# Kernel optimization log

Hardware: AMD Instinct MI355X
Metric: run time of the kernel (lower is better)

Reference implementation:

```python
import jax, jax.numpy as jnp
import numpy as np

B, NX, W, DX, DY, D, H, P = 8, 512, 16, 1536, 1024, 768, 12, 8


def setup_inputs() -> dict:
    key = jax.random.key(0)
    ks = jax.random.split(key, 12)
    r = lambda k, s: jax.random.normal(k, s, dtype=jnp.float32) * 0.02
    return {
        "x": jax.random.normal(ks[0], (B, NX, DX), jnp.float32),
        "y": jax.random.normal(ks[1], (B, NX * W, DY), jnp.float32),
        "Wx": r(ks[2], (DX, D)), "bx": jnp.zeros((D,), jnp.float32),
        "Wy": r(ks[3], (DY, D)), "by": jnp.zeros((D,), jnp.float32),
        "prompt": r(ks[4], (1, P, D)),
        "Wq": r(ks[5], (D, D)), "bq": jnp.zeros((D,), jnp.float32),
        "Wk": r(ks[6], (D, D)), "bk": jnp.zeros((D,), jnp.float32),
        "Wv": r(ks[7], (D, D)), "bv": jnp.zeros((D,), jnp.float32),
        "Wo": r(ks[8], (D, D)), "bo": jnp.zeros((D,), jnp.float32),
        "ln_g": jnp.ones((D,), jnp.float32), "ln_b": jnp.zeros((D,), jnp.float32),
    }


def _l2n(f, eps=1e-6):
    return f / (jnp.linalg.norm(f, axis=-1, keepdims=True) + eps)


def reference(x, y, Wx, bx, Wy, by, prompt, Wq, bq, Wk, bk, Wv, bv, Wo, bo, ln_g, ln_b):
    dh = D // H
    scale = 1.0 / jnp.sqrt(jnp.float32(dh))
    xp = _l2n(x @ Wx + bx)            # [B,NX,D]
    yp = _l2n(y @ Wy + by)            # [B,NX*W,D]
    # In the original, only normalized_output[:,0:1] is kept per window, and
    # per-query attention is independent, so only query index 0 contributes.
    q = ((xp[:, 0] @ Wq) + bq).reshape(B, H, dh) * scale   # [B,H,dh]
    yw = yp.reshape(B, NX, W, D)                            # 16-token windows
    k = ((yw @ Wk) + bk).reshape(B, NX, W, H, dh)
    v = ((yw @ Wv) + bv).reshape(B, NX, W, H, dh)
    s = jnp.einsum('bhd,bnwhd->bhnw', q, k)                # [B,H,NX,W]
    a = jax.nn.softmax(s, axis=-1)
    ctx = jnp.einsum('bhnw,bnwhd->bnhd', a, v).reshape(B, NX, D)
    o = ctx @ Wo + bo                                      # attn out_proj
    mu = jnp.mean(o, axis=-1, keepdims=True)
    var = jnp.var(o, axis=-1, keepdims=True)
    normed = (o - mu) / jnp.sqrt(var + 1e-6) * ln_g + ln_b  # [B,NX,D]
    blocks = jnp.concatenate(
        [normed[:, :, None, :],
         jnp.broadcast_to(prompt[:, None], (B, NX, P, D))], axis=2)  # [B,NX,1+P,D]
    return blocks.reshape(B, NX * (1 + P), D)
```

## Files before the change

### kernel.cpp

```cpp
#include <hip/hip_runtime.h>
#include <stdint.h>

#define BQ 8
#define NXQ 512
#define WQ 16
#define DXQ 1536
#define DYQ 1024
#define DQ 768
#define HQ 12
#define PQ 8
#define MY 65536
#define BN_ROWS 4096

typedef __attribute__((ext_vector_type(8))) short short8;
typedef __attribute__((ext_vector_type(4))) float f32x4;
typedef unsigned short ushort_t;
typedef unsigned int uint_t;

__device__ __forceinline__ ushort_t f2bf(float f) {
  uint_t u = __float_as_uint(f);
  u += 0x7FFFu + ((u >> 16) & 1u);
  return (ushort_t)(u >> 16);
}
__device__ __forceinline__ float bf2f(ushort_t h) {
  return __uint_as_float(((uint_t)h) << 16);
}
__device__ __forceinline__ void gload_lds16(const void* g, void* l) {
  __builtin_amdgcn_global_load_lds(
      (__attribute__((address_space(1))) unsigned int*)(g),
      (__attribute__((address_space(3))) unsigned int*)(l), 16, 0, 0);
}

__global__ void k_conv(const float* __restrict__ y, const float* __restrict__ Wy,
                       const float* __restrict__ Wv, const float* __restrict__ Wo,
                       ushort_t* __restrict__ ybf, ushort_t* __restrict__ WyT,
                       ushort_t* __restrict__ WvT, ushort_t* __restrict__ WoT,
                       float* __restrict__ rowsq, float* __restrict__ oS12,
                       float* __restrict__ xw) {
  const int gstride = gridDim.x * blockDim.x;
  const int g0 = blockIdx.x * blockDim.x + threadIdx.x;
  const int NY8 = MY * DYQ / 8;
  for (int i = g0; i < NY8; i += gstride) {
    const float4* s = (const float4*)(y + (size_t)i * 8);
    float4 f0 = s[0], f1 = s[1];
    short8 hv;
    hv[0] = (short)f2bf(f0.x); hv[1] = (short)f2bf(f0.y);
    hv[2] = (short)f2bf(f0.z); hv[3] = (short)f2bf(f0.w);
    hv[4] = (short)f2bf(f1.x); hv[5] = (short)f2bf(f1.y);
    hv[6] = (short)f2bf(f1.z); hv[7] = (short)f2bf(f1.w);
    *(short8*)(ybf + (size_t)i * 8) = hv;
  }
  for (int i = g0; i < MY; i += gstride) rowsq[i] = 0.f;
  for (int i = g0; i < 2 * BN_ROWS; i += gstride) oS12[i] = 0.f;
  for (int i = g0; i < BQ * DQ; i += gstride) xw[i] = 0.f;
  const int N1 = DQ * DYQ;
  const int N2 = DQ * DQ;
  const int total = N1 + 2 * N2;
  for (int i = g0; i < total; i += gstride) {
    if (i < N1) {
      int n = i / DYQ, k = i - n * DYQ;
      WyT[i] = f2bf(Wy[k * DQ + n]);
    } else if (i < N1 + N2) {
      int j = i - N1;
      int n = j / DQ, k = j - n * DQ;
      WvT[j] = f2bf(Wv[k * DQ + n]);
    } else {
      int j = i - N1 - N2;
      int n = j / DQ, k = j - n * DQ;
      WoT[j] = f2bf(Wo[k * DQ + n]);
    }
  }
}

__global__ __launch_bounds__(128) void k_q1(const float* __restrict__ x,
                                            const float* __restrict__ Wx,
                                            const float* __restrict__ bx,
                                            float* __restrict__ xw) {
  const int b = blockIdx.x, c = blockIdx.y * 128 + threadIdx.x;
  const int kc = blockIdx.z;
  const float* xr = x + (size_t)b * NXQ * DXQ + kc * 192;
  const float* wp = Wx + (size_t)kc * 192 * DQ + c;
  float acc = (kc == 0) ? bx[c] : 0.f;
  for (int k = 0; k < 192; ++k) acc += xr[k] * wp[(size_t)k * DQ];
  atomicAdd(&xw[b * DQ + c], acc);
}

__global__ __launch_bounds__(128) void k_q2(const float* __restrict__ xw,
                                            const float* __restrict__ Wq,
                                            const float* __restrict__ bq,
                                            float* __restrict__ qv) {
  const int b = blockIdx.x, c = blockIdx.y * 128 + threadIdx.x;
  const float* xr = xw + b * DQ;
  float acc = 0.f, ss = 0.f;
  for (int k = 0; k < DQ; ++k) {
    float v = xr[k];
    acc += v * Wq[(size_t)k * DQ + c];
    ss += v * v;
  }
  const float inv = 1.0f / (sqrtf(ss) + 1e-6f);
  qv[b * DQ + c] = (acc * inv + bq[c]) * 0.125f;
}

__global__ void k_q3(const float* __restrict__ Wk, const float* __restrict__ bk,
                     const float* __restrict__ qv, float* __restrict__ qk,
                     float* __restrict__ cQ) {
  const int bh = blockIdx.x;
  const int b = bh / HQ, h = bh - b * HQ;
  const int tid = threadIdx.x;
  const float* q = qv + b * DQ + h * 64;
#pragma unroll
  for (int j = 0; j < 3; ++j) {
    int dd = tid + j * 256;
    float acc = 0.f;
    for (int j2 = 0; j2 < 64; ++j2) acc += Wk[(size_t)dd * DQ + h * 64 + j2] * q[j2];
    qk[(size_t)bh * DQ + dd] = acc;
  }
  if (tid == 0) {
    float acc = 0.f;
    for (int j2 = 0; j2 < 64; ++j2) acc += q[j2] * bk[h * 64 + j2];
    cQ[bh] = acc;
  }
}

__global__ __launch_bounds__(512, 1) void k_gemm_yp(const ushort_t* __restrict__ ybf,
                                                    const ushort_t* __restrict__ WyT,
                                                    const float* __restrict__ by,
                                                    ushort_t* __restrict__ z,
                                                    float* __restrict__ rowsqg) {
  __shared__ __align__(16) char smem[131072 + 1024];
  float* rowsq_l = (float*)(smem + 131072);
  const int tid = threadIdx.x, lane = tid & 63, wv = tid >> 6;
  const int wvM = wv >> 2, wvN = wv & 3;
  const int g = blockIdx.x;
  const int m = (g / 24) * 8 + (g & 7);
  const int n = (g >> 3) % 3;
  const int mBase = m * 256, nBase = n * 256;
  if (tid < 256) rowsq_l[tid] = 0.f;

  const int sr = lane >> 2;
  const int sc = (lane & 3) ^ ((lane >> 3) & 3);
  const ushort_t* aQ[2]; const ushort_t* bQ[2];
  int qDst[2];
#pragma unroll
  for (int j = 0; j < 2; ++j) {
    int r = wv * 32 + j * 16 + sr;
    aQ[j] = ybf + (size_t)(mBase + r) * DYQ + sc * 8;
    bQ[j] = WyT + (size_t)(nBase + r) * DYQ + sc * 8;
    qDst[j] = (wv * 32 + j * 16) * 64;
  }
  const int q = lane >> 4;
  const int fsw = ((lane & 15) >> 1) & 3;
  int aFr[8], bFr[4];
#pragma unroll
  for (int mf = 0; mf < 8; ++mf) {
    int r = wvM * 128 + mf * 16 + (lane & 15);
    aFr[mf] = r * 64 + ((q ^ fsw) << 4);
  }
#pragma unroll
  for (int nf = 0; nf < 4; ++nf) {
    int r = wvN * 64 + nf * 16 + (lane & 15);
    bFr[nf] = 16384 + r * 64 + ((q ^ fsw) << 4);
  }

#define YP_STAGE(pp)                                                           \
  {                                                                            \
    char* db = smem + ((pp) & 3) * 32768;                                      \
    const int koff = ((pp) >> 1) * 64 + ((pp) & 1) * 32;                       \
    _Pragma("unroll") for (int j = 0; j < 2; ++j)                              \
        gload_lds16(aQ[j] + koff, db + qDst[j]);                               \
    _Pragma("unroll") for (int j = 0; j < 2; ++j)                              \
        gload_lds16(bQ[j] + koff, db + 16384 + qDst[j]);                       \
  }

  f32x4 acc[8][4] = {};
  YP_STAGE(0);
  YP_STAGE(1);
  YP_STAGE(2);
  asm volatile("s_waitcnt vmcnt(8)" ::: "memory");
  __builtin_amdgcn_s_barrier();
  __builtin_amdgcn_sched_barrier(0);

  for (int t = 0; t < 16; ++t) {
#pragma unroll
    for (int ks = 0; ks < 2; ++ks) {
      const int p = 2 * t + ks;
      const char* cb = smem + (p & 3) * 32768;
      short8 af[8], bf[4];
#pragma unroll
      for (int mf = 0; mf < 8; ++mf) af[mf] = *(const short8*)(cb + aFr[mf]);
#pragma unroll
      for (int nf = 0; nf < 4; ++nf) bf[nf] = *(const short8*)(cb + bFr[nf]);
      if (p <= 28) YP_STAGE(p + 3);
      asm volatile("s_waitcnt lgkmcnt(0)" ::: "memory");
      __builtin_amdgcn_sched_barrier(0);
      __builtin_amdgcn_s_setprio(1);
#pragma unroll
      for (int nf = 0; nf < 4; ++nf)
#pragma unroll
        for (int mf = 0; mf < 8; ++mf)
          acc[mf][nf] = __builtin_amdgcn_mfma_f32_16x16x32_bf16(af[mf], bf[nf],
                                                                acc[mf][nf], 0, 0, 0);
      __builtin_amdgcn_s_setprio(0);
      __builtin_amdgcn_sched_barrier(0);
      if (p <= 28) {
        asm volatile("s_waitcnt vmcnt(8)" ::: "memory");
      } else if (p == 29) {
        asm volatile("s_waitcnt vmcnt(4)" ::: "memory");
      } else {
        asm volatile("s_waitcnt vmcnt(0)" ::: "memory");
      }
      __builtin_amdgcn_s_barrier();
      __builtin_amdgcn_sched_barrier(0);
    }
  }
  __syncthreads();

  float byv[4];
#pragma unroll
  for (int nf = 0; nf < 4; ++nf) byv[nf] = by[nBase + wvN * 64 + nf * 16 + (lane & 15)];
#pragma unroll
  for (int mf = 0; mf < 8; ++mf) {
#pragma unroll
    for (int rr = 0; rr < 4; ++rr) {
      int row_l = wvM * 128 + mf * 16 + (lane >> 4) * 4 + rr;
      float ss = 0.f;
#pragma unroll
      for (int nf = 0; nf < 4; ++nf) {
        float zv = acc[mf][nf][rr] + byv[nf];
        ss += zv * zv;
        int col_l = wvN * 64 + nf * 16 + (lane & 15);
        *(ushort_t*)(smem + row_l * 512 + col_l * 2) = f2bf(zv);
      }
#pragma unroll
      for (int o = 1; o < 16; o <<= 1) ss += __shfl_xor(ss, o, 64);
      if ((lane & 15) == 0) atomicAdd(&rowsq_l[row_l], ss);
    }
  }
  __syncthreads();
  if (tid < 256) atomicAdd(&rowsqg[mBase + tid], rowsq_l[tid]);
#pragma unroll
  for (int it = 0; it < 16; ++it) {
    int row = it * 16 + (tid >> 5);
    int ch = tid & 31;
    uint4 v = *(const uint4*)(smem + row * 512 + ch * 16);
    *(uint4*)(z + (size_t)(mBase + row) * DQ + nBase + ch * 8) = v;
  }
}

__global__ __launch_bounds__(256) void k_attn(const ushort_t* __restrict__ z,
                                              const float* __restrict__ rowsqg,
                                              const float* __restrict__ qk,
                                              const float* __restrict__ cQ,
                                              ushort_t* __restrict__ p) {
  __shared__ __align__(16) char smem[16 * 1552 + 192 * 4 * 2 + 64];
  float* s_l = (float*)(smem + 16 * 1552);
  float* a_l = s_l + 192;
  float* inv_l = a_l + 192;
  const int bn = blockIdx.x, b = bn >> 9;
  const int tid = threadIdx.x;
  if (tid < 16) inv_l[tid] = 1.0f / (sqrtf(rowsqg[bn * 16 + tid]) + 1e-6f);
  for (int j = tid; j < 16 * 96; j += 256) {
    int w = j / 96, ch = j - w * 96;
    *(short8*)(smem + w * 1552 + ch * 16) =
        *(const short8*)(z + ((size_t)bn * 16 + w) * DQ + ch * 8);
  }
  __syncthreads();
  if (tid < 192) {
    int h = tid >> 4, w = tid & 15;
    const float4* qkp = (const float4*)(qk + (size_t)(b * HQ + h) * DQ);
    float acc = 0.f;
    const char* yrow = smem + w * 1552;
    for (int dc = 0; dc < 192; ++dc) {
      float4 q4 = qkp[dc];
      uint2 hh = *(const uint2*)(yrow + dc * 8);
      acc += q4.x * bf2f((ushort_t)(hh.x & 0xffff));
      acc += q4.y * bf2f((ushort_t)(hh.x >> 16));
      acc += q4.z * bf2f((ushort_t)(hh.y & 0xffff));
      acc += q4.w * bf2f((ushort_t)(hh.y >> 16));
    }
    s_l[tid] = acc * inv_l[w] + cQ[b * HQ + h];
  }
  __syncthreads();
  if (tid < 12) {
    float mx = -1e30f;
#pragma unroll
    for (int w = 0; w < 16; ++w) mx = fmaxf(mx, s_l[tid * 16 + w]);
    float sm = 0.f, ev[16];
#pragma unroll
    for (int w = 0; w < 16; ++w) {
      ev[w] = __expf(s_l[tid * 16 + w] - mx);
      sm += ev[w];
    }
    float rden = 1.0f / sm;
#pragma unroll
    for (int w = 0; w < 16; ++w) a_l[tid * 16 + w] = ev[w] * rden * inv_l[w];
  }
  __syncthreads();
  float zr[16][3];
#pragma unroll
  for (int w = 0; w < 16; ++w)
#pragma unroll
    for (int i = 0; i < 3; ++i)
      zr[w][i] = bf2f(*(const ushort_t*)(smem + w * 1552 + (tid + i * 256) * 2));
  for (int h = 0; h < HQ; ++h) {
    float acc0 = 0.f, acc1 = 0.f, acc2 = 0.f;
#pragma unroll
    for (int w = 0; w < 16; ++w) {
      float aw = a_l[h * 16 + w];
      acc0 += aw * zr[w][0];
      acc1 += aw * zr[w][1];
      acc2 += aw * zr[w][2];
    }
    size_t base = ((size_t)bn * HQ + h) * DQ + tid;
    p[base] = f2bf(acc0);
    p[base + 256] = f2bf(acc1);
    p[base + 512] = f2bf(acc2);
  }
}

#define PV_TSZ 24576
__global__ __launch_bounds__(256) void k_gemm_pv(const ushort_t* __restrict__ p,
                                                 const ushort_t* __restrict__ WvT,
                                                 const float* __restrict__ bv,
                                                 ushort_t* __restrict__ ctx) {
  __shared__ __align__(16) char smem[3 * PV_TSZ];
  const int tid = threadIdx.x, lane = tid & 63, wv = tid >> 6;
  const int wvM = wv >> 1, wvN = wv & 1;
  const int mBase = blockIdx.x * 128, h = blockIdx.y;
  const int l8 = lane >> 3;
  const int c8 = (lane & 7) ^ (l8 & 7);
  const ushort_t* aSrc[4]; const ushort_t* bSrc[2];
  int aDst[4], bDst[2];
#pragma unroll
  for (int j = 0; j < 4; ++j) {
    int r = wv * 32 + j * 8 + l8;
    aSrc[j] = p + ((size_t)(mBase + r) * HQ + h) * DQ + c8 * 8;
    aDst[j] = (wv * 32 + j * 8) * 128;
  }
#pragma unroll
  for (int j = 0; j < 2; ++j) {
    int r = wv * 16 + j * 8 + l8;
    bSrc[j] = WvT + (size_t)(h * 64 + r) * DQ + c8 * 8;
    bDst[j] = 16384 + (wv * 16 + j * 8) * 128;
  }
  const int q = lane >> 4;
  int aRowB[4], aSw[4], bRowB[2], bSw[2];
#pragma unroll
  for (int mf = 0; mf < 4; ++mf) {
    int r = wvM * 64 + mf * 16 + (lane & 15);
    aRowB[mf] = r * 128; aSw[mf] = r & 7;
  }
#pragma unroll
  for (int nf = 0; nf < 2; ++nf) {
    int r = wvN * 32 + nf * 16 + (lane & 15);
    bRowB[nf] = 16384 + r * 128; bSw[nf] = r & 7;
  }
#define PV_STAGE(dbuf, t)                                                      \
  {                                                                            \
    char* db = smem + (dbuf) * PV_TSZ;                                         \
    _Pragma("unroll") for (int j = 0; j < 4; ++j)                              \
        gload_lds16(aSrc[j] + (t) * 64, db + aDst[j]);                         \
    _Pragma("unroll") for (int j = 0; j < 2; ++j)                              \
        gload_lds16(bSrc[j] + (t) * 64, db + bDst[j]);                         \
  }
  f32x4 acc[4][2] = {};
  PV_STAGE(0, 0);
  PV_STAGE(1, 1);
  int bR = 0, bS = 2;
  for (int t = 0; t < 12; ++t) {
    if (t < 11) {
      asm volatile("s_waitcnt vmcnt(6)" ::: "memory");
    } else {
      asm volatile("s_waitcnt vmcnt(0)" ::: "memory");
    }
    __builtin_amdgcn_s_barrier();
    __builtin_amdgcn_sched_barrier(0);
    if (t + 2 < 12) PV_STAGE(bS, t + 2);
    const char* cur = smem + bR * PV_TSZ;
#pragma unroll
    for (int ks = 0; ks < 2; ++ks) {
      short8 af[4], bf[2];
#pragma unroll
      for (int mf = 0; mf < 4; ++mf)
        af[mf] = *(const short8*)(cur + aRowB[mf] + (((ks * 4 + q) ^ aSw[mf]) << 4));
#pragma unroll
      for (int nf = 0; nf < 2; ++nf)
        bf[nf] = *(const short8*)(cur + bRowB[nf] + (((ks * 4 + q) ^ bSw[nf]) << 4));
#pragma unroll
      for (int nf = 0; nf < 2; ++nf)
#pragma unroll
        for (int mf = 0; mf < 4; ++mf)
          acc[mf][nf] = __builtin_amdgcn_mfma_f32_16x16x32_bf16(af[mf], bf[nf],
                                                                acc[mf][nf], 0, 0, 0);
    }
    bR = (bR == 2) ? 0 : bR + 1;
    bS = (bS == 2) ? 0 : bS + 1;
  }
#pragma unroll
  for (int nf = 0; nf < 2; ++nf) {
    int col = h * 64 + wvN * 32 + nf * 16 + (lane & 15);
    float bvv = bv[col];
#pragma unroll
    for (int mf = 0; mf < 4; ++mf)
#pragma unroll
      for (int rr = 0; rr < 4; ++rr) {
        int row = mBase + wvM * 64 + mf * 16 + (lane >> 4) * 4 + rr;
        ctx[(size_t)row * DQ + col] = f2bf(acc[mf][nf][rr] + bvv);
      }
  }
}

__global__ __launch_bounds__(256) void k_gemm_o(const ushort_t* __restrict__ ctx,
                                                const ushort_t* __restrict__ WoT,
                                                const float* __restrict__ bo,
                                                float* __restrict__ o,
                                                float* __restrict__ oS12) {
  __shared__ __align__(16) char smem[3 * PV_TSZ];
  const int tid = threadIdx.x, lane = tid & 63, wv = tid >> 6;
  const int wvM = wv >> 1, wvN = wv & 1;
  const int mBase = blockIdx.x * 128, nBase = blockIdx.y * 64;
  const int l8 = lane >> 3;
  const int c8 = (lane & 7) ^ (l8 & 7);
  const ushort_t* aSrc[4]; const ushort_t* bSrc[2];
  int aDst[4], bDst[2];
#pragma unroll
  for (int j = 0; j < 4; ++j) {
    int r = wv * 32 + j * 8 + l8;
    aSrc[j] = ctx + (size_t)(mBase + r) * DQ + c8 * 8;
    aDst[j] = (wv * 32 + j * 8) * 128;
  }
#pragma unroll
  for (int j = 0; j < 2; ++j) {
    int r = wv * 16 + j * 8 + l8;
    bSrc[j] = WoT + (size_t)(nBase + r) * DQ + c8 * 8;
    bDst[j] = 16384 + (wv * 16 + j * 8) * 128;
  }
  const int q = lane >> 4;
  int aRowB[4], aSw[4], bRowB[2], bSw[2];
#pragma unroll
  for (int mf = 0; mf < 4; ++mf) {
    int r = wvM * 64 + mf * 16 + (lane & 15);
    aRowB[mf] = r * 128; aSw[mf] = r & 7;
  }
#pragma unroll
  for (int nf = 0; nf < 2; ++nf) {
    int r = wvN * 32 + nf * 16 + (lane & 15);
    bRowB[nf] = 16384 + r * 128; bSw[nf] = r & 7;
  }
  f32x4 acc[4][2] = {};
#define O_STAGE(dbuf, t)                                                       \
  {                                                                            \
    char* db = smem + (dbuf) * PV_TSZ;                                         \
    _Pragma("unroll") for (int j = 0; j < 4; ++j)                              \
        gload_lds16(aSrc[j] + (t) * 64, db + aDst[j]);                         \
    _Pragma("unroll") for (int j = 0; j < 2; ++j)                              \
        gload_lds16(bSrc[j] + (t) * 64, db + bDst[j]);                         \
  }
  O_STAGE(0, 0);
  O_STAGE(1, 1);
  int bR = 0, bS = 2;
  for (int t = 0; t < 12; ++t) {
    if (t < 11) {
      asm volatile("s_waitcnt vmcnt(6)" ::: "memory");
    } else {
      asm volatile("s_waitcnt vmcnt(0)" ::: "memory");
    }
    __builtin_amdgcn_s_barrier();
    __builtin_amdgcn_sched_barrier(0);
    if (t + 2 < 12) O_STAGE(bS, t + 2);
    const char* cur = smem + bR * PV_TSZ;
#pragma unroll
    for (int ks = 0; ks < 2; ++ks) {
      short8 af[4], bf[2];
#pragma unroll
      for (int mf = 0; mf < 4; ++mf)
        af[mf] = *(const short8*)(cur + aRowB[mf] + (((ks * 4 + q) ^ aSw[mf]) << 4));
#pragma unroll
      for (int nf = 0; nf < 2; ++nf)
        bf[nf] = *(const short8*)(cur + bRowB[nf] + (((ks * 4 + q) ^ bSw[nf]) << 4));
#pragma unroll
      for (int nf = 0; nf < 2; ++nf)
#pragma unroll
        for (int mf = 0; mf < 4; ++mf)
          acc[mf][nf] = __builtin_amdgcn_mfma_f32_16x16x32_bf16(af[mf], bf[nf],
                                                                acc[mf][nf], 0, 0, 0);
    }
    bR = (bR == 2) ? 0 : bR + 1;
    bS = (bS == 2) ? 0 : bS + 1;
  }
  float bo0 = bo[nBase + wvN * 32 + (lane & 15)];
  float bo1 = bo[nBase + wvN * 32 + 16 + (lane & 15)];
#pragma unroll
  for (int mf = 0; mf < 4; ++mf)
#pragma unroll
    for (int rr = 0; rr < 4; ++rr) {
      int row = mBase + wvM * 64 + mf * 16 + (lane >> 4) * 4 + rr;
      float z0 = acc[mf][0][rr] + bo0;
      float z1 = acc[mf][1][rr] + bo1;
      o[(size_t)row * DQ + nBase + wvN * 32 + (lane & 15)] = z0;
      o[(size_t)row * DQ + nBase + wvN * 32 + 16 + (lane & 15)] = z1;
      float s1 = z0 + z1, s2 = z0 * z0 + z1 * z1;
#pragma unroll
      for (int ofs = 1; ofs < 16; ofs <<= 1) {
        s1 += __shfl_xor(s1, ofs, 64);
        s2 += __shfl_xor(s2, ofs, 64);
      }
      if ((lane & 15) == 0) {
        atomicAdd(&oS12[row], s1);
        atomicAdd(&oS12[BN_ROWS + row], s2);
      }
    }
}

__global__ __launch_bounds__(256) void k_out(const float* __restrict__ o,
                                             const float* __restrict__ oS12,
                                             const float* __restrict__ ln_g,
                                             const float* __restrict__ ln_b,
                                             const float* __restrict__ prompt,
                                             float* __restrict__ out) {
  const int row = blockIdx.x;
  const int tid = threadIdx.x;
  float mu = oS12[row] * (1.0f / DQ);
  float va = oS12[BN_ROWS + row] * (1.0f / DQ) - mu * mu;
  float rstd = rsqrtf(va + 1e-6f);
  int b = row >> 9, n = row & 511;
  size_t obase = ((size_t)b * (NXQ * (PQ + 1)) + (size_t)n * (PQ + 1)) * DQ;
#pragma unroll
  for (int j = 0; j < 3; ++j) {
    int col = tid + j * 256;
    out[obase + col] = (o[(size_t)row * DQ + col] - mu) * rstd * ln_g[col] + ln_b[col];
  }
#pragma unroll
  for (int pi = 0; pi < PQ; ++pi)
#pragma unroll
    for (int j = 0; j < 3; ++j) {
      int col = tid + j * 256;
      out[obase + (size_t)(1 + pi) * DQ + col] = prompt[pi * DQ + col];
    }
}

extern "C" void kernel_launch(void* const* d_in, const int* in_sizes, int n_in,
                              void* d_out, int out_size, void* d_ws, size_t ws_size,
                              hipStream_t stream) {
  (void)in_sizes; (void)n_in; (void)out_size; (void)ws_size;
  const float* x    = (const float*)d_in[0];
  const float* y    = (const float*)d_in[1];
  const float* Wx   = (const float*)d_in[2];
  const float* bx   = (const float*)d_in[3];
  const float* Wy   = (const float*)d_in[4];
  const float* by   = (const float*)d_in[5];
  const float* prom = (const float*)d_in[6];
  const float* Wq   = (const float*)d_in[7];
  const float* bq   = (const float*)d_in[8];
  const float* Wk   = (const float*)d_in[9];
  const float* bk   = (const float*)d_in[10];
  const float* Wv   = (const float*)d_in[11];
  const float* bv   = (const float*)d_in[12];
  const float* Wo   = (const float*)d_in[13];
  const float* bo   = (const float*)d_in[14];
  const float* lng  = (const float*)d_in[15];
  const float* lnb  = (const float*)d_in[16];
  float* out = (float*)d_out;
  char* ws = (char*)d_ws;

  size_t oWyT = 0;
  size_t oWvT = oWyT + (size_t)DQ * DYQ * 2;
  size_t oWoT = oWvT + (size_t)DQ * DQ * 2;
  size_t oXw  = oWoT + (size_t)DQ * DQ * 2;
  size_t oQ   = oXw + (size_t)BQ * DQ * 4 + 256;
  size_t oQK  = oQ + (size_t)BQ * DQ * 4;
  size_t oC   = oQK + (size_t)BQ * HQ * DQ * 4;
  size_t oRq  = oC + 1024;
  size_t oS   = oRq + (size_t)MY * 4;
  size_t oYbf = oS + (size_t)2 * BN_ROWS * 4;
  size_t oZ   = oYbf + (size_t)MY * DYQ * 2;
  size_t oP   = oYbf;
  size_t oCtx = oYbf + (size_t)BN_ROWS * HQ * DQ * 2;
  size_t oO   = oZ;

  ushort_t* WyT = (ushort_t*)(ws + oWyT);
  ushort_t* WvT = (ushort_t*)(ws + oWvT);
  ushort_t* WoT = (ushort_t*)(ws + oWoT);
  float* xw  = (float*)(ws + oXw);
  float* qv  = (float*)(ws + oQ);
  float* qk  = (float*)(ws + oQK);
  float* cQ  = (float*)(ws + oC);
  float* rowsq = (float*)(ws + oRq);
  float* oS12  = (float*)(ws + oS);
  ushort_t* ybf  = (ushort_t*)(ws + oYbf);
  ushort_t* zbuf = (ushort_t*)(ws + oZ);
  ushort_t* p    = (ushort_t*)(ws + oP);
  ushort_t* ctx  = (ushort_t*)(ws + oCtx);
  float* obuf    = (float*)(ws + oO);

  k_conv<<<dim3(4096), dim3(256), 0, stream>>>(y, Wy, Wv, Wo, ybf, WyT, WvT, WoT,
                                               rowsq, oS12, xw);
  k_q1<<<dim3(BQ, 6, 8), dim3(128), 0, stream>>>(x, Wx, bx, xw);
  k_q2<<<dim3(BQ, 6), dim3(128), 0, stream>>>(xw, Wq, bq, qv);
  k_q3<<<dim3(BQ * HQ), dim3(256), 0, stream>>>(Wk, bk, qv, qk, cQ);
  k_gemm_yp<<<dim3(768), dim3(512), 0, stream>>>(ybf, WyT, by, zbuf, rowsq);
  k_attn<<<dim3(BN_ROWS), dim3(256), 0, stream>>>(zbuf, rowsq, qk, cQ, p);
  k_gemm_pv<<<dim3(BN_ROWS / 128, HQ), dim3(256), 0, stream>>>(p, WvT, bv, ctx);
  k_gemm_o<<<dim3(BN_ROWS / 128, DQ / 64), dim3(256), 0, stream>>>(ctx, WoT, bo, obuf, oS12);
  k_out<<<dim3(BN_ROWS), dim3(256), 0, stream>>>(obuf, oS12, lng, lnb, prom, out);
}
```

Baseline: 445.5 us.

## Shrink yp GEMM tile to 128x256 with 3-stage pipeline for higher occupancy

The y-projection GEMM moves from 256x256 tiles with a 4-buffer, 64-wide K pipeline to 128x256 tiles with a 3-buffer, 32-wide K pipeline. Shared memory drops from about 129KB to about 73KB and launch bounds allow several blocks per CU, so two blocks can share a CU and hide latency; the grid doubles to 1536 blocks. The cost is lower data reuse per tile (each B tile is loaded twice as often) and more barrier iterations per block.

```diff
diff --git a/kernel.cpp b/kernel.cpp
--- a/kernel.cpp
+++ b/kernel.cpp
@@ -122,96 +122,83 @@
   }
 }
 
-__global__ __launch_bounds__(512, 1) void k_gemm_yp(const ushort_t* __restrict__ ybf,
+__global__ __launch_bounds__(512, 4) void k_gemm_yp(const ushort_t* __restrict__ ybf,
                                                     const ushort_t* __restrict__ WyT,
                                                     const float* __restrict__ by,
                                                     ushort_t* __restrict__ z,
                                                     float* __restrict__ rowsqg) {
-  __shared__ __align__(16) char smem[131072 + 1024];
-  float* rowsq_l = (float*)(smem + 131072);
+  __shared__ __align__(16) char smem[3 * 24576 + 512];
+  float* rowsq_l = (float*)(smem + 3 * 24576);
   const int tid = threadIdx.x, lane = tid & 63, wv = tid >> 6;
   const int wvM = wv >> 2, wvN = wv & 3;
   const int g = blockIdx.x;
   const int m = (g / 24) * 8 + (g & 7);
   const int n = (g >> 3) % 3;
-  const int mBase = m * 256, nBase = n * 256;
-  if (tid < 256) rowsq_l[tid] = 0.f;
-
-  const int sr = lane >> 2;
-  const int sc = (lane & 3) ^ ((lane >> 3) & 3);
-  const ushort_t* aQ[2]; const ushort_t* bQ[2];
-  int qDst[2];
-#pragma unroll
-  for (int j = 0; j < 2; ++j) {
-    int r = wv * 32 + j * 16 + sr;
-    aQ[j] = ybf + (size_t)(mBase + r) * DYQ + sc * 8;
-    bQ[j] = WyT + (size_t)(nBase + r) * DYQ + sc * 8;
-    qDst[j] = (wv * 32 + j * 16) * 64;
-  }
+  const int mBase = m * 128, nBase = n * 256;
+  if (tid < 128) rowsq_l[tid] = 0.f;
+
+  const int srow = tid >> 2;
+  const int schk = (tid & 3) ^ ((tid >> 3) & 3);
+  const ushort_t* aS = ybf + (size_t)(mBase + srow) * DYQ + schk * 8;
+  const ushort_t* bS0 = WyT + (size_t)(nBase + srow) * DYQ + schk * 8;
+  const ushort_t* bS1 = WyT + (size_t)(nBase + 128 + srow) * DYQ + schk * 8;
+  const int sDst = tid * 16;
   const int q = lane >> 4;
   const int fsw = ((lane & 15) >> 1) & 3;
-  int aFr[8], bFr[4];
-#pragma unroll
-  for (int mf = 0; mf < 8; ++mf) {
-    int r = wvM * 128 + mf * 16 + (lane & 15);
+  int aFr[4], bFr[4];
+#pragma unroll
+  for (int mf = 0; mf < 4; ++mf) {
+    int r = wvM * 64 + mf * 16 + (lane & 15);
     aFr[mf] = r * 64 + ((q ^ fsw) << 4);
   }
 #pragma unroll
   for (int nf = 0; nf < 4; ++nf) {
     int r = wvN * 64 + nf * 16 + (lane & 15);
-    bFr[nf] = 16384 + r * 64 + ((q ^ fsw) << 4);
+    bFr[nf] = 8192 + r * 64 + ((q ^ fsw) << 4);
   }
 
 #define YP_STAGE(pp)                                                           \
   {                                                                            \
-    char* db = smem + ((pp) & 3) * 32768;                                      \
-    const int koff = ((pp) >> 1) * 64 + ((pp) & 1) * 32;                       \
-    _Pragma("unroll") for (int j = 0; j < 2; ++j)                              \
-        gload_lds16(aQ[j] + koff, db + qDst[j]);                               \
-    _Pragma("unroll") for (int j = 0; j < 2; ++j)                              \
-        gload_lds16(bQ[j] + koff, db + 16384 + qDst[j]);                       \
-  }
-
-  f32x4 acc[8][4] = {};
+    char* db = smem + ((pp) % 3) * 24576;                                      \
+    const int koff = (pp) * 32;                                                \
+    gload_lds16(aS + koff, db + sDst);                                         \
+    gload_lds16(bS0 + koff, db + 8192 + sDst);                                 \
+    gload_lds16(bS1 + koff, db + 16384 + sDst);                                \
+  }
+
+  f32x4 acc[4][4] = {};
   YP_STAGE(0);
   YP_STAGE(1);
-  YP_STAGE(2);
-  asm volatile("s_waitcnt vmcnt(8)" ::: "memory");
+  asm volatile("s_waitcnt vmcnt(3)" ::: "memory");
   __builtin_amdgcn_s_barrier();
   __builtin_amdgcn_sched_barrier(0);
 
-  for (int t = 0; t < 16; ++t) {
-#pragma unroll
-    for (int ks = 0; ks < 2; ++ks) {
-      const int p = 2 * t + ks;
-      const char* cb = smem + (p & 3) * 32768;
-      short8 af[8], bf[4];
-#pragma unroll
-      for (int mf = 0; mf < 8; ++mf) af[mf] = *(const short8*)(cb + aFr[mf]);
-#pragma unroll
-      for (int nf = 0; nf < 4; ++nf) bf[nf] = *(const short8*)(cb + bFr[nf]);
-      if (p <= 28) YP_STAGE(p + 3);
-      asm volatile("s_waitcnt lgkmcnt(0)" ::: "memory");
-      __builtin_amdgcn_sched_barrier(0);
-      __builtin_amdgcn_s_setprio(1);
-#pragma unroll
-      for (int nf = 0; nf < 4; ++nf)
-#pragma unroll
-        for (int mf = 0; mf < 8; ++mf)
-          acc[mf][nf] = __builtin_amdgcn_mfma_f32_16x16x32_bf16(af[mf], bf[nf],
-                                                                acc[mf][nf], 0, 0, 0);
-      __builtin_amdgcn_s_setprio(0);
-      __builtin_amdgcn_sched_barrier(0);
-      if (p <= 28) {
-        asm volatile("s_waitcnt vmcnt(8)" ::: "memory");
-      } else if (p == 29) {
-        asm volatile("s_waitcnt vmcnt(4)" ::: "memory");
-      } else {
-        asm volatile("s_waitcnt vmcnt(0)" ::: "memory");
-      }
-      __builtin_amdgcn_s_barrier();
-      __builtin_amdgcn_sched_barrier(0);
-    }
+  for (int p = 0; p < 32; ++p) {
+    const char* cb = smem + (p % 3) * 24576;
+    short8 af[4], bf[4];
+#pragma unroll
+    for (int mf = 0; mf < 4; ++mf) af[mf] = *(const short8*)(cb + aFr[mf]);
+#pragma unroll
+    for (int nf = 0; nf < 4; ++nf) bf[nf] = *(const short8*)(cb + bFr[nf]);
+    if (p <= 29) YP_STAGE(p + 2);
+    asm volatile("s_waitcnt lgkmcnt(0)" ::: "memory");
+    __builtin_amdgcn_sched_barrier(0);
+    __builtin_amdgcn_s_setprio(1);
+#pragma unroll
+    for (int nf = 0; nf < 4; ++nf)
+#pragma unroll
+      for (int mf = 0; mf < 4; ++mf)
+        acc[mf][nf] = __builtin_amdgcn_mfma_f32_16x16x32_bf16(af[mf], bf[nf],
+                                                              acc[mf][nf], 0, 0, 0);
+    __builtin_amdgcn_s_setprio(0);
+    __builtin_amdgcn_sched_barrier(0);
+    if (p <= 29) {
+      asm volatile("s_waitcnt vmcnt(3)" ::: "memory");
+    } else {
+      asm volatile("s_waitcnt vmcnt(0)" ::: "memory");
+    }
+    __builtin_amdgcn_s_barrier();
+    __builtin_amdgcn_sched_barrier(0);
   }
   __syncthreads();
 
@@ -219,10 +206,10 @@
 #pragma unroll
   for (int nf = 0; nf < 4; ++nf) byv[nf] = by[nBase + wvN * 64 + nf * 16 + (lane & 15)];
 #pragma unroll
-  for (int mf = 0; mf < 8; ++mf) {
+  for (int mf = 0; mf < 4; ++mf) {
 #pragma unroll
     for (int rr = 0; rr < 4; ++rr) {
-      int row_l = wvM * 128 + mf * 16 + (lane >> 4) * 4 + rr;
+      int row_l = wvM * 64 + mf * 16 + (lane >> 4) * 4 + rr;
       float ss = 0.f;
 #pragma unroll
       for (int nf = 0; nf < 4; ++nf) {
@@ -237,9 +224,9 @@
     }
   }
   __syncthreads();
-  if (tid < 256) atomicAdd(&rowsqg[mBase + tid], rowsq_l[tid]);
-#pragma unroll
-  for (int it = 0; it < 16; ++it) {
+  if (tid < 128) atomicAdd(&rowsqg[mBase + tid], rowsq_l[tid]);
+#pragma unroll
+  for (int it = 0; it < 8; ++it) {
     int row = it * 16 + (tid >> 5);
     int ch = tid & 31;
     uint4 v = *(const uint4*)(smem + row * 512 + ch * 16);
@@ -598,7 +585,7 @@
   k_q1<<<dim3(BQ, 6, 8), dim3(128), 0, stream>>>(x, Wx, bx, xw);
   k_q2<<<dim3(BQ, 6), dim3(128), 0, stream>>>(xw, Wq, bq, qv);
   k_q3<<<dim3(BQ * HQ), dim3(256), 0, stream>>>(Wk, bk, qv, qk, cQ);
-  k_gemm_yp<<<dim3(768), dim3(512), 0, stream>>>(ybf, WyT, by, zbuf, rowsq);
+  k_gemm_yp<<<dim3(1536), dim3(512), 0, stream>>>(ybf, WyT, by, zbuf, rowsq);
   k_attn<<<dim3(BN_ROWS), dim3(256), 0, stream>>>(zbuf, rowsq, qk, cQ, p);
   k_gemm_pv<<<dim3(BN_ROWS / 128, HQ), dim3(256), 0, stream>>>(p, WvT, bv, ctx);
   k_gemm_o<<<dim3(BN_ROWS / 128, DQ / 64), dim3(256), 0, stream>>>(ctx, WoT, bo, obuf, oS12);
```

After: 441.2 us (median of 2 runs). No clear change (-1.0%).

## Fuse fp32-to-bf16 conversion of y into the projection GEMM A-load

Applied to the files above, without the earlier changes.

Removes the separate pass that converted the whole 256MB fp32 y tensor to bf16 in a workspace buffer. The GEMM now loads fp32 y rows straight into registers, packs them to bf16 and writes them to swizzled LDS, with a register double-buffer and a pipeline depth cut from three stages to two. This saves one full read and a write/read of the bf16 copy. In exchange the GEMM reads the A operand at twice the bytes and adds VALU pack work and register pressure inside the main loop. Workspace offsets are rearranged to match.

```diff
diff --git a/kernel.cpp b/kernel.cpp
--- a/kernel.cpp
+++ b/kernel.cpp
@@ -25,31 +25,22 @@
 __device__ __forceinline__ float bf2f(ushort_t h) {
   return __uint_as_float(((uint_t)h) << 16);
 }
+__device__ __forceinline__ uint_t pkbf(float a, float b) {
+  return (uint_t)f2bf(a) | ((uint_t)f2bf(b) << 16);
+}
 __device__ __forceinline__ void gload_lds16(const void* g, void* l) {
   __builtin_amdgcn_global_load_lds(
       (__attribute__((address_space(1))) unsigned int*)(g),
       (__attribute__((address_space(3))) unsigned int*)(l), 16, 0, 0);
 }
 
-__global__ void k_conv(const float* __restrict__ y, const float* __restrict__ Wy,
-                       const float* __restrict__ Wv, const float* __restrict__ Wo,
-                       ushort_t* __restrict__ ybf, ushort_t* __restrict__ WyT,
+__global__ void k_conv(const float* __restrict__ Wy, const float* __restrict__ Wv,
+                       const float* __restrict__ Wo, ushort_t* __restrict__ WyT,
                        ushort_t* __restrict__ WvT, ushort_t* __restrict__ WoT,
                        float* __restrict__ rowsq, float* __restrict__ oS12,
                        float* __restrict__ xw) {
   const int gstride = gridDim.x * blockDim.x;
   const int g0 = blockIdx.x * blockDim.x + threadIdx.x;
-  const int NY8 = MY * DYQ / 8;
-  for (int i = g0; i < NY8; i += gstride) {
-    const float4* s = (const float4*)(y + (size_t)i * 8);
-    float4 f0 = s[0], f1 = s[1];
-    short8 hv;
-    hv[0] = (short)f2bf(f0.x); hv[1] = (short)f2bf(f0.y);
-    hv[2] = (short)f2bf(f0.z); hv[3] = (short)f2bf(f0.w);
-    hv[4] = (short)f2bf(f1.x); hv[5] = (short)f2bf(f1.y);
-    hv[6] = (short)f2bf(f1.z); hv[7] = (short)f2bf(f1.w);
-    *(short8*)(ybf + (size_t)i * 8) = hv;
-  }
   for (int i = g0; i < MY; i += gstride) rowsq[i] = 0.f;
   for (int i = g0; i < 2 * BN_ROWS; i += gstride) oS12[i] = 0.f;
   for (int i = g0; i < BQ * DQ; i += gstride) xw[i] = 0.f;
@@ -122,7 +113,7 @@
   }
 }
 
-__global__ __launch_bounds__(512, 1) void k_gemm_yp(const ushort_t* __restrict__ ybf,
+__global__ __launch_bounds__(512, 1) void k_gemm_yp(const float* __restrict__ y,
                                                     const ushort_t* __restrict__ WyT,
                                                     const float* __restrict__ by,
                                                     ushort_t* __restrict__ z,
@@ -137,16 +128,20 @@
   const int mBase = m * 256, nBase = n * 256;
   if (tid < 256) rowsq_l[tid] = 0.f;
 
+  const int arow = tid >> 1, akh = tid & 1;
+  const float* aLd = y + (size_t)(mBase + arow) * DYQ + akh * 16;
+  const int afw = (arow >> 1) & 3;
+  const int aWr0 = arow * 64 + (((akh * 2 + 0) ^ afw) << 4);
+  const int aWr1 = arow * 64 + (((akh * 2 + 1) ^ afw) << 4);
   const int sr = lane >> 2;
   const int sc = (lane & 3) ^ ((lane >> 3) & 3);
-  const ushort_t* aQ[2]; const ushort_t* bQ[2];
-  int qDst[2];
+  const ushort_t* bQ[2];
+  int bDst[2];
 #pragma unroll
   for (int j = 0; j < 2; ++j) {
     int r = wv * 32 + j * 16 + sr;
-    aQ[j] = ybf + (size_t)(mBase + r) * DYQ + sc * 8;
     bQ[j] = WyT + (size_t)(nBase + r) * DYQ + sc * 8;
-    qDst[j] = (wv * 32 + j * 16) * 64;
+    bDst[j] = 16384 + (wv * 32 + j * 16) * 64;
   }
   const int q = lane >> 4;
   const int fsw = ((lane & 15) >> 1) & 3;
@@ -162,21 +157,39 @@
     bFr[nf] = 16384 + r * 64 + ((q ^ fsw) << 4);
   }
 
-#define YP_STAGE(pp)                                                           \
+#define YP_LOADA(dst, pp)                                                      \
+  {                                                                            \
+    const float4* ap = (const float4*)(aLd + (pp) * 32);                       \
+    dst[0] = ap[0]; dst[1] = ap[1]; dst[2] = ap[2]; dst[3] = ap[3];            \
+  }
+#define YP_ISSUE_B(pp)                                                         \
   {                                                                            \
     char* db = smem + ((pp) & 3) * 32768;                                      \
-    const int koff = ((pp) >> 1) * 64 + ((pp) & 1) * 32;                       \
-    _Pragma("unroll") for (int j = 0; j < 2; ++j)                              \
-        gload_lds16(aQ[j] + koff, db + qDst[j]);                               \
-    _Pragma("unroll") for (int j = 0; j < 2; ++j)                              \
-        gload_lds16(bQ[j] + koff, db + 16384 + qDst[j]);                       \
+    gload_lds16(bQ[0] + (pp) * 32, db + bDst[0]);                              \
+    gload_lds16(bQ[1] + (pp) * 32, db + bDst[1]);                              \
+  }
+#define YP_WRITEA(src, pp)                                                     \
+  {                                                                            \
+    char* dw = smem + ((pp) & 3) * 32768;                                      \
+    uint4 w0, w1;                                                              \
+    w0.x = pkbf(src[0].x, src[0].y); w0.y = pkbf(src[0].z, src[0].w);          \
+    w0.z = pkbf(src[1].x, src[1].y); w0.w = pkbf(src[1].z, src[1].w);          \
+    w1.x = pkbf(src[2].x, src[2].y); w1.y = pkbf(src[2].z, src[2].w);          \
+    w1.z = pkbf(src[3].x, src[3].y); w1.w = pkbf(src[3].z, src[3].w);          \
+    *(uint4*)(dw + aWr0) = w0;                                                 \
+    *(uint4*)(dw + aWr1) = w1;                                                 \
   }
 
   f32x4 acc[8][4] = {};
-  YP_STAGE(0);
-  YP_STAGE(1);
-  YP_STAGE(2);
-  asm volatile("s_waitcnt vmcnt(8)" ::: "memory");
+  float4 rA0[4], rA1[4];
+  YP_LOADA(rA0, 0);
+  YP_ISSUE_B(0);
+  YP_LOADA(rA1, 1);
+  YP_ISSUE_B(1);
+  __builtin_amdgcn_sched_barrier(0);
+  asm volatile("s_waitcnt vmcnt(6)" ::: "memory");
+  YP_WRITEA(rA0, 0);
+  asm volatile("s_waitcnt lgkmcnt(0)" ::: "memory");
   __builtin_amdgcn_s_barrier();
   __builtin_amdgcn_sched_barrier(0);
 
@@ -190,7 +203,19 @@
       for (int mf = 0; mf < 8; ++mf) af[mf] = *(const short8*)(cb + aFr[mf]);
 #pragma unroll
       for (int nf = 0; nf < 4; ++nf) bf[nf] = *(const short8*)(cb + bFr[nf]);
-      if (p <= 28) YP_STAGE(p + 3);
+      if (p + 2 <= 31) {
+        if (ks == 0) { YP_LOADA(rA0, p + 2); } else { YP_LOADA(rA1, p + 2); }
+        YP_ISSUE_B(p + 2);
+      }
+      __builtin_amdgcn_sched_barrier(0);
+      if (p <= 29) {
+        asm volatile("s_waitcnt vmcnt(6)" ::: "memory");
+      } else {
+        asm volatile("s_waitcnt vmcnt(0)" ::: "memory");
+      }
+      if (p <= 30) {
+        if (ks == 0) { YP_WRITEA(rA1, p + 1); } else { YP_WRITEA(rA0, p + 1); }
+      }
       asm volatile("s_waitcnt lgkmcnt(0)" ::: "memory");
       __builtin_amdgcn_sched_barrier(0);
       __builtin_amdgcn_s_setprio(1);
@@ -202,13 +227,6 @@
                                                                 acc[mf][nf], 0, 0, 0);
       __builtin_amdgcn_s_setprio(0);
       __builtin_amdgcn_sched_barrier(0);
-      if (p <= 28) {
-        asm volatile("s_waitcnt vmcnt(8)" ::: "memory");
-      } else if (p == 29) {
-        asm volatile("s_waitcnt vmcnt(4)" ::: "memory");
-      } else {
-        asm volatile("s_waitcnt vmcnt(0)" ::: "memory");
-      }
       __builtin_amdgcn_s_barrier();
       __builtin_amdgcn_sched_barrier(0);
     }
@@ -572,10 +590,9 @@
   size_t oC   = oQK + (size_t)BQ * HQ * DQ * 4;
   size_t oRq  = oC + 1024;
   size_t oS   = oRq + (size_t)MY * 4;
-  size_t oYbf = oS + (size_t)2 * BN_ROWS * 4;
-  size_t oZ   = oYbf + (size_t)MY * DYQ * 2;
-  size_t oP   = oYbf;
-  size_t oCtx = oYbf + (size_t)BN_ROWS * HQ * DQ * 2;
+  size_t oZ   = oS + (size_t)2 * BN_ROWS * 4;
+  size_t oP   = oZ + (size_t)MY * DQ * 2;
+  size_t oCtx = oP + (size_t)BN_ROWS * HQ * DQ * 2;
   size_t oO   = oZ;
 
   ushort_t* WyT = (ushort_t*)(ws + oWyT);
@@ -587,18 +604,17 @@
   float* cQ  = (float*)(ws + oC);
   float* rowsq = (float*)(ws + oRq);
   float* oS12  = (float*)(ws + oS);
-  ushort_t* ybf  = (ushort_t*)(ws + oYbf);
   ushort_t* zbuf = (ushort_t*)(ws + oZ);
   ushort_t* p    = (ushort_t*)(ws + oP);
   ushort_t* ctx  = (ushort_t*)(ws + oCtx);
   float* obuf    = (float*)(ws + oO);
 
-  k_conv<<<dim3(4096), dim3(256), 0, stream>>>(y, Wy, Wv, Wo, ybf, WyT, WvT, WoT,
+  k_conv<<<dim3(1024), dim3(256), 0, stream>>>(Wy, Wv, Wo, WyT, WvT, WoT,
                                                rowsq, oS12, xw);
   k_q1<<<dim3(BQ, 6, 8), dim3(128), 0, stream>>>(x, Wx, bx, xw);
   k_q2<<<dim3(BQ, 6), dim3(128), 0, stream>>>(xw, Wq, bq, qv);
   k_q3<<<dim3(BQ * HQ), dim3(256), 0, stream>>>(Wk, bk, qv, qk, cQ);
-  k_gemm_yp<<<dim3(768), dim3(512), 0, stream>>>(ybf, WyT, by, zbuf, rowsq);
+  k_gemm_yp<<<dim3(768), dim3(512), 0, stream>>>(y, WyT, by, zbuf, rowsq);
   k_attn<<<dim3(BN_ROWS), dim3(256), 0, stream>>>(zbuf, rowsq, qk, cQ, p);
   k_gemm_pv<<<dim3(BN_ROWS / 128, HQ), dim3(256), 0, stream>>>(p, WvT, bv, ctx);
   k_gemm_o<<<dim3(BN_ROWS / 128, DQ / 64), dim3(256), 0, stream>>>(ctx, WoT, bo, obuf, oS12);
```

New measurement: 488.4 us. +9.6%, slower.
